# Kernel tuning notes

Measured on AMD Instinct MI355X. Metric: run time of the kernel, lower is better.

Reference implementation:

```python
import jax, jax.numpy as jnp
import numpy as np
from jax import lax

SD = 16          # sample_duration
STRIDE = 16      # feat_stride
SCALES = (4, 8, 16)
RATIOS = (0.5, 1.0, 2.0)
PRE_NMS = 1000   # proposals kept before NMS (TEST config)
POST_NMS = 128   # proposals kept after NMS
NMS_TH = 0.7


def _anchors2d():
    base = 16.0
    ctr = (base - 1.0) / 2.0
    out = []
    for r in RATIOS:
        ws = np.round(np.sqrt(base * base / r))
        hs = np.round(ws * r)
        for s in SCALES:
            w, h = ws * s, hs * s
            out.append([ctr - (w - 1) / 2, ctr - (h - 1) / 2,
                        ctr + (w - 1) / 2, ctr + (h - 1) / 2])
    return np.asarray(out, np.float32)                       # (9, 4)


def _anchors3d():
    # tube anchors: (x1, y1, t1, x2, y2, t2), durations [SD, SD/2, SD/4]
    a2 = _anchors2d()
    out = []
    for d in (SD, SD // 2, SD // 4):
        for a in a2:
            out.append([a[0], a[1], 0.0, a[2], a[3], d - 1.0])
    return np.asarray(out, np.float32)                       # (27, 6)


def _shifted(anchors, H, W):
    k = anchors.shape[-1]
    sx = jnp.arange(W, dtype=jnp.float32) * STRIDE
    sy = jnp.arange(H, dtype=jnp.float32) * STRIDE
    if k == 4:
        sh = jnp.stack(jnp.broadcast_arrays(sx[None, :], sy[:, None],
                                            sx[None, :], sy[:, None]), -1)
    else:
        z = jnp.zeros((H, W), jnp.float32)
        sh = jnp.stack(jnp.broadcast_arrays(sx[None, :], sy[:, None], z,
                                            sx[None, :], sy[:, None], z), -1)
    return (sh[:, :, None, :] + jnp.asarray(anchors)[None, None]).reshape(-1, k)


def _decode(anchors, deltas):
    # deltas layout: (d_ctr..., d_logsize...); works for 2D (k=4) and 3D (k=6)
    nd = anchors.shape[-1] // 2
    lo, hi = anchors[..., :nd], anchors[..., nd:]
    size = hi - lo + 1.0
    ctr = lo + 0.5 * (size - 1.0)
    pctr = deltas[..., :nd] * size + ctr
    psize = jnp.exp(deltas[..., nd:]) * size
    return jnp.concatenate([pctr - 0.5 * (psize - 1.0),
                            pctr + 0.5 * (psize - 1.0)], -1)


def _iou(b, boxes):
    # b: (k,), boxes: (N, k); area/volume IoU with +1 pixel convention
    nd = boxes.shape[-1] // 2
    lo = jnp.maximum(b[:nd], boxes[:, :nd])
    hi = jnp.minimum(b[nd:], boxes[:, nd:])
    inter = jnp.prod(jnp.maximum(hi - lo + 1.0, 0.0), -1)
    va = jnp.prod(b[nd:] - b[:nd] + 1.0)
    vb = jnp.prod(boxes[:, nd:] - boxes[:, :nd] + 1.0, -1)
    return inter / (va + vb - inter)


def _nms(boxes):
    # boxes already sorted by descending score; greedy NMS, fixed output size
    N = boxes.shape[0]

    def body(i, c):
        supp, keep = c
        idx = jnp.argmax(~supp)                 # first unsuppressed box
        keep = keep.at[i].set(idx.astype(jnp.int32))
        supp = supp | (_iou(boxes[idx], boxes) > NMS_TH)
        supp = supp.at[idx].set(True)
        return supp, keep

    _, keep = lax.fori_loop(0, POST_NMS, body,
                            (jnp.zeros(N, bool), jnp.zeros(POST_NMS, jnp.int32)))
    return keep


def _proposals(scores, deltas, anchors, maxs):
    # scores (B,N), deltas (B,N,k), anchors (N,k), maxs (B,1,k)
    boxes = jnp.clip(_decode(anchors[None], deltas), 0.0, maxs)
    _, idx = lax.top_k(scores, PRE_NMS)
    bx = jnp.take_along_axis(boxes, idx[..., None], axis=1)   # (B,PRE,k)
    keep = jax.vmap(_nms)(bx)                                 # (B,POST)
    sel = jnp.take_along_axis(bx, keep[..., None], axis=1)    # (B,POST,k)
    bidx = jnp.broadcast_to(
        jnp.arange(sel.shape[0], dtype=sel.dtype)[:, None, None],
        sel.shape[:2] + (1,))
    return lax.stop_gradient(jnp.concatenate([bidx, sel], -1))


def setup_inputs() -> dict:
    k = jax.random.split(jax.random.key(0), 8)
    s = 0.01
    return {
        "base_feat": jax.random.normal(k[0], (1, 256, 16, 32, 32), jnp.float32),
        "im_info": jnp.array([[512.0, 512.0, 1.0]], jnp.float32),
        "gt_boxes": jax.random.uniform(k[1], (1, 5, 7), jnp.float32) * 100.0,
        "gt_rois": jax.random.uniform(k[2], (1, 5, 16, 5), jnp.float32) * 100.0,
        "W_conv": jax.random.normal(k[3], (512, 256, 3, 3, 3), jnp.float32) * s,
        "b_conv": jnp.zeros((512,), jnp.float32),
        "W_cls": jax.random.normal(k[4], (54, 512), jnp.float32) * s,
        "b_cls": jnp.zeros((54,), jnp.float32),
        "W_bbox": jax.random.normal(k[5], (162, 512), jnp.float32) * s,
        "b_bbox": jnp.zeros((162,), jnp.float32),
        "W_cls16": jax.random.normal(k[6], (18, 512), jnp.float32) * s,
        "b_cls16": jnp.zeros((18,), jnp.float32),
        "W_bbox16": jax.random.normal(k[7], (36, 512), jnp.float32) * s,
        "b_bbox16": jnp.zeros((36,), jnp.float32),
    }


def reference(base_feat, im_info, gt_boxes, gt_rois, W_conv, b_conv,
              W_cls, b_cls, W_bbox, b_bbox, W_cls16, b_cls16,
              W_bbox16, b_bbox16):
    B, _, T, H, W = base_feat.shape
    # RPN_Conv: 3x3x3 Conv3d + ReLU
    conv1 = jax.nn.relu(
        lax.conv_general_dilated(base_feat, W_conv, (1, 1, 1), "SAME",
                                 dimension_numbers=("NCDHW", "OIDHW", "NCDHW"))
        + b_conv[None, :, None, None, None])
    # 1x1x1 score / bbox heads (3D)
    cls3 = jnp.einsum("bcthw,oc->bothw", conv1, W_cls) + b_cls[None, :, None, None, None]
    bbox3 = jnp.einsum("bcthw,oc->bothw", conv1, W_bbox) + b_bbox[None, :, None, None, None]
    # permute(0,1,3,4,2).mean(4) == mean over the temporal axis
    feat2 = conv1.mean(axis=2)
    cls2 = jnp.einsum("bchw,oc->bohw", feat2, W_cls16) + b_cls16[None, :, None, None]
    bbox2 = jnp.einsum("bchw,oc->bohw", feat2, W_bbox16) + b_bbox16[None, :, None, None]
    # reshape(x,2) + softmax over dim 1; fg prob is the second half of channels
    fg3 = jax.nn.softmax(cls3.reshape(B, 2, 27, T, H, W), axis=1)[:, 1]  # (B,27,T,H,W)
    fg2 = jax.nn.softmax(cls2.reshape(B, 2, 9, H, W), axis=1)[:, 1]      # (B,9,H,W)
    # proposal layers consume detached tensors (torch .data)
    fg3, fg2, bbox3d, bbox2d = map(lax.stop_gradient, (fg3, fg2, bbox3, bbox2))
    # flatten position-major (h, w, anchor)
    sc3 = fg3.mean(axis=2).transpose(0, 2, 3, 1).reshape(B, -1)
    dl3 = bbox3d.mean(axis=2).reshape(B, 27, 6, H, W).transpose(0, 3, 4, 1, 2).reshape(B, -1, 6)
    sc2 = fg2.transpose(0, 2, 3, 1).reshape(B, -1)
    dl2 = bbox2d.reshape(B, 9, 4, H, W).transpose(0, 3, 4, 1, 2).reshape(B, -1, 4)
    imh, imw = im_info[:, 0][:, None], im_info[:, 1][:, None]
    sdm = jnp.full_like(imw, SD - 1.0)
    max3 = jnp.stack([imw - 1, imh - 1, sdm, imw - 1, imh - 1, sdm], -1)  # (B,1,6)
    max2 = jnp.stack([imw - 1, imh - 1, imw - 1, imh - 1], -1)            # (B,1,4)
    rois = _proposals(sc3, dl3, _shifted(_anchors3d(), H, W), max3)       # (B,POST,7)
    rois16 = _proposals(sc2, dl2, _shifted(_anchors2d(), H, W), max2)     # (B,POST,5)
    z = jnp.zeros((), jnp.float32)  # eval mode: all RPN losses are 0
    return rois, rois16, z, z, z, z
```

## Files before the change

kernel.cpp:

```cpp
#include <hip/hip_runtime.h>
#include <hip/hip_bf16.h>
#include <cfloat>
#include <cstdint>


#define T_DIM 16
#define H_DIM 32
#define W_DIM 32
#define NVOX  (T_DIM*H_DIM*W_DIM)
#define HW    (H_DIM*W_DIM)
#define CIN   256
#define COUT  512
#define PRE_NMS 1000
#define POST_NMS 128
#define NMS_TH 0.7f

typedef __attribute__((ext_vector_type(8))) short v8s;
typedef __attribute__((ext_vector_type(4))) float v4f;
typedef __attribute__((ext_vector_type(4))) int v4i;

#define MFMA_B16(A,B,C) __builtin_amdgcn_mfma_f32_16x16x32_bf16(A,B,C,0,0,0)

__device__ __forceinline__ short f2bf(float x) {
    unsigned u = __float_as_uint(x);
    u += 0x7FFFu + ((u >> 16) & 1u);
    return (short)(u >> 16);
}
__device__ __forceinline__ float bf2f(short s) {
    return __uint_as_float(((unsigned)(unsigned short)s) << 16);
}

__constant__ float c_ws[3] = {23.f, 16.f, 11.f};
__constant__ float c_hs[3] = {12.f, 16.f, 22.f};
__constant__ float c_sc[3] = {4.f, 8.f, 16.f};
__constant__ float c_depth[3] = {16.f, 8.f, 4.f};

__global__ void k_split_w(const float* __restrict__ W, short* __restrict__ A0,
                          short* __restrict__ A1, short* __restrict__ A2) {
    int i = blockIdx.x * 256 + threadIdx.x;
    int c7 = i & 7;
    int o = (i >> 3) & 511;
    int ko = (i >> 12) & 31;
    int tap = i >> 17;
    int c = ko * 8 + c7;
    float x = W[(o * 256 + c) * 27 + tap];
    short h = f2bf(x); float r = x - bf2f(h);
    short m = f2bf(r); float r2 = r - bf2f(m);
    short l = f2bf(r2);
    A0[i] = h; A1[i] = m; A2[i] = l;
}

__global__ void k_build_wcomb(const float* __restrict__ Wcls, const float* __restrict__ Wbb,
                              float* __restrict__ Wc) {
    int i = blockIdx.x * 256 + threadIdx.x;
    int o = i & 255;
    int c = i >> 8;
    float v = 0.f;
    if (o < 54) v = Wcls[o * 512 + c];
    else if (o < 216) v = Wbb[(o - 54) * 512 + c];
    Wc[i] = v;
}

#define SPLIT2(X0, X1, OH, OM, OL) {                                          \
    unsigned u0_ = __float_as_uint(X0), u1_ = __float_as_uint(X1);            \
    OH = (int)__builtin_amdgcn_perm(u1_, u0_, 0x07060302u);                   \
    float h0_ = __uint_as_float(u0_ & 0xFFFF0000u);                           \
    float h1_ = __uint_as_float(u1_ & 0xFFFF0000u);                           \
    float r0_ = (X0) - h0_, r1_ = (X1) - h1_;                                 \
    unsigned v0_ = __float_as_uint(r0_), v1_ = __float_as_uint(r1_);          \
    OM = (int)__builtin_amdgcn_perm(v1_, v0_, 0x07060302u);                   \
    float m0_ = __uint_as_float(v0_ & 0xFFFF0000u);                           \
    float m1_ = __uint_as_float(v1_ & 0xFFFF0000u);                           \
    float s0_ = r0_ - m0_, s1_ = r1_ - m1_;                                   \
    OL = (int)__builtin_amdgcn_perm(__float_as_uint(s1_),                     \
                                    __float_as_uint(s0_), 0x07060302u);       \
}

__global__ void k_split_i(const float* __restrict__ I, v4i* __restrict__ Ih,
                          v4i* __restrict__ Im, v4i* __restrict__ Il) {
    int t = blockIdx.x * 256 + threadIdx.x;
    int vox = t & 16383;
    int ck8 = t >> 14;
    const float* ip = I + ((size_t)ck8 << 3) * NVOX + vox;
    int h[4], m[4], l[4];
#pragma unroll
    for (int j = 0; j < 4; ++j) {
        float x0 = ip[(size_t)(2 * j) * NVOX];
        float x1 = ip[(size_t)(2 * j + 1) * NVOX];
        SPLIT2(x0, x1, h[j], m[j], l[j]);
    }
    Ih[t] = (v4i){h[0], h[1], h[2], h[3]};
    Im[t] = (v4i){m[0], m[1], m[2], m[3]};
    Il[t] = (v4i){l[0], l[1], l[2], l[3]};
}

#define CV_SHIFT(TAP) {                                                       \
    int kt_ = (TAP) / 9 - 1, kh_ = ((TAP) / 3) % 3 - 1, kw_ = (TAP) % 3 - 1;  \
    int tt_ = bt + kt_, hh_ = bh + kh_, ww_ = bw + kw_;                       \
    bVal = ((unsigned)tt_ < 16u) && ((unsigned)hh_ < 32u) && ((unsigned)ww_ < 32u); \
    bOff = bVal ? ((tt_ << 10) + (hh_ << 5) + ww_) : 0;                       \
}

#define CV_LOAD_BP(CK8B) {                                                    \
    const size_t bidx_ = (((size_t)((CK8B) + skh * 2)) << 14) + bOff;         \
    nh0 = Ih[bidx_]; nh1 = Ih[bidx_ + NVOX];                                  \
    nm0 = Im[bidx_]; nm1 = Im[bidx_ + NVOX];                                  \
    nl0 = Il[bidx_]; nl1 = Il[bidx_ + NVOX];                                  \
}

#define CV_SELECT_B() {                                                       \
    v4i z_ = (v4i){0, 0, 0, 0};                                               \
    pbh0 = bVal ? nh0 : z_; pbh1 = bVal ? nh1 : z_;                           \
    pbm0 = bVal ? nm0 : z_; pbm1 = bVal ? nm1 : z_;                           \
    pbl0 = bVal ? nl0 : z_; pbl1 = bVal ? nl1 : z_;                           \
}

#define LOAD_ASET(S) {                                                        \
    const size_t aB_ = (((size_t)((S) >> 3) * 32 + (((S) & 7) << 2)) << 12) + aLane; \
    ah0 = *(const v8s*)(A0 + aB_);       ah1 = *(const v8s*)(A0 + aB_ + 128); \
    ah2 = *(const v8s*)(A0 + aB_ + 256); ah3 = *(const v8s*)(A0 + aB_ + 384); \
    am0 = *(const v8s*)(A1 + aB_);       am1 = *(const v8s*)(A1 + aB_ + 128); \
    am2 = *(const v8s*)(A1 + aB_ + 256); am3 = *(const v8s*)(A1 + aB_ + 384); \
    al0 = *(const v8s*)(A2 + aB_);       al1 = *(const v8s*)(A2 + aB_ + 128); \
    al2 = *(const v8s*)(A2 + aB_ + 256); al3 = *(const v8s*)(A2 + aB_ + 384); \
}

#define COMPUTE() {                                                           \
    _Pragma("unroll")                                                         \
    for (int j = 0; j < 4; ++j) {                                             \
        v8s bb = *(const v8s*)(&Bsh[0][uB + j * 16]);                         \
        v8s bm = *(const v8s*)(&Bsh[1][uB + j * 16]);                         \
        v8s bl = *(const v8s*)(&Bsh[2][uB + j * 16]);                         \
        v4f a;                                                                \
        a = acc[0][j];                                                        \
        a = MFMA_B16(ah0, bb, a); a = MFMA_B16(ah0, bm, a);                   \
        a = MFMA_B16(am0, bb, a); a = MFMA_B16(ah0, bl, a);                   \
        a = MFMA_B16(am0, bm, a); a = MFMA_B16(al0, bb, a);                   \
        acc[0][j] = a;                                                        \
        a = acc[1][j];                                                        \
        a = MFMA_B16(ah1, bb, a); a = MFMA_B16(ah1, bm, a);                   \
        a = MFMA_B16(am1, bb, a); a = MFMA_B16(ah1, bl, a);                   \
        a = MFMA_B16(am1, bm, a); a = MFMA_B16(al1, bb, a);                   \
        acc[1][j] = a;                                                        \
        a = acc[2][j];                                                        \
        a = MFMA_B16(ah2, bb, a); a = MFMA_B16(ah2, bm, a);                   \
        a = MFMA_B16(am2, bb, a); a = MFMA_B16(ah2, bl, a);                   \
        a = MFMA_B16(am2, bm, a); a = MFMA_B16(al2, bb, a);                   \
        acc[2][j] = a;                                                        \
        a = acc[3][j];                                                        \
        a = MFMA_B16(ah3, bb, a); a = MFMA_B16(ah3, bm, a);                   \
        a = MFMA_B16(am3, bb, a); a = MFMA_B16(ah3, bl, a);                   \
        a = MFMA_B16(am3, bm, a); a = MFMA_B16(al3, bb, a);                   \
        acc[3][j] = a;                                                        \
    }                                                                         \
}

__global__ __launch_bounds__(256) void k_conv3d_mfma(
        const v4i* __restrict__ Ih, const v4i* __restrict__ Im,
        const v4i* __restrict__ Il, const short* __restrict__ A0,
        const short* __restrict__ A1, const short* __restrict__ A2,
        const float* __restrict__ bias, float* __restrict__ O) {
    __shared__ v4i Bsh[3][512];
    const int tid = threadIdx.x;
    const int o0 = blockIdx.y * 128;
    const int v0 = blockIdx.x * 128;
    const int lane = tid & 63;
    const int wv = tid >> 6;
    const int quad = lane >> 4, m16 = lane & 15;
    const int wo = (wv >> 1) * 64;
    const int wvx = (wv & 1) * 64;

    const int sa_o = tid >> 1, skh = tid & 1;
    const int uW0 = (skh * 2) * 128 + sa_o;
    const int uW1 = (skh * 2 + 1) * 128 + sa_o;

    const int vbase = v0 + sa_o;
    const int bt = vbase >> 10, bh = (vbase >> 5) & 31, bw = vbase & 31;

    const int uB = quad * 128 + wvx + m16;

    const size_t aLane = ((size_t)(o0 + wo + m16) << 3) + ((size_t)quad << 12);

    v4f acc[4][4];
#pragma unroll
    for (int i = 0; i < 4; i++)
#pragma unroll
        for (int j = 0; j < 4; j++) acc[i][j] = (v4f){0.f, 0.f, 0.f, 0.f};

    int bOff, bVal;
    v4i pbh0, pbh1, pbm0, pbm1, pbl0, pbl1;
    v4i nh0, nh1, nm0, nm1, nl0, nl1;
    v8s ah0, ah1, ah2, ah3, am0, am1, am2, am3, al0, al1, al2, al3;

    CV_SHIFT(0);
    CV_LOAD_BP(0);
    CV_SELECT_B();

    for (int s = 0; s < 216; ++s) {
        __syncthreads();
        Bsh[0][uW0] = pbh0; Bsh[0][uW1] = pbh1;
        Bsh[1][uW0] = pbm0; Bsh[1][uW1] = pbm1;
        Bsh[2][uW0] = pbl0; Bsh[2][uW1] = pbl1;
        __syncthreads();
        LOAD_ASET(s);
        {
            int s1 = s + 1;
            if (s1 < 216) {
                if ((s1 & 7) == 0) CV_SHIFT(s1 >> 3);
                CV_LOAD_BP((s1 & 7) << 2);
            }
        }
        COMPUTE();
        if (s + 1 < 216) CV_SELECT_B();
    }

#pragma unroll
    for (int i = 0; i < 4; ++i) {
#pragma unroll
        for (int r = 0; r < 4; ++r) {
            int o = o0 + wo + i * 16 + quad * 4 + r;
            float bo = bias[o];
            float* dst = O + (size_t)o * NVOX + v0 + wvx + m16;
#pragma unroll
            for (int j = 0; j < 4; ++j)
                dst[j * 16] = fmaxf(acc[i][j][r] + bo, 0.f);
        }
    }
}

__global__ __launch_bounds__(256) void k_gemm_logits3(const float* __restrict__ conv1,
                                                      const float* __restrict__ Wc,
                                                      float* __restrict__ L) {
    __shared__ float As[16][64];
    __shared__ float Bs[16][64];
    const int tid = threadIdx.x;
    const int o0 = blockIdx.y * 64;
    const int v0 = blockIdx.x * 64;
    const int ty = tid >> 4, tx = tid & 15;
    const int c_l = tid >> 4, e4 = (tid & 15) << 2;

    float acc[4][4];
#pragma unroll
    for (int i = 0; i < 4; i++)
#pragma unroll
        for (int j = 0; j < 4; j++) acc[i][j] = 0.f;

    for (int ck = 0; ck < 512; ck += 16) {
        __syncthreads();
        *(float4*)(&As[c_l][e4]) = *(const float4*)(Wc + ((size_t)(ck + c_l) << 8) + o0 + e4);
        *(float4*)(&Bs[c_l][e4]) = *(const float4*)(conv1 + ((size_t)(ck + c_l) << 14) + v0 + e4);
        __syncthreads();
#pragma unroll
        for (int k = 0; k < 16; ++k) {
            float a[4], b[4];
            *(float4*)(a) = *(const float4*)(&As[k][ty * 4]);
            *(float4*)(b) = *(const float4*)(&Bs[k][tx * 4]);
#pragma unroll
            for (int i = 0; i < 4; i++)
#pragma unroll
                for (int j = 0; j < 4; j++)
                    acc[i][j] = fmaf(a[i], b[j], acc[i][j]);
        }
    }
#pragma unroll
    for (int i = 0; i < 4; i++) {
        float* dst = L + (size_t)(o0 + ty * 4 + i) * NVOX + v0 + tx * 4;
        *(float4*)(dst) = *(const float4*)(&acc[i][0]);
    }
}

__global__ void k_sc3(const float* __restrict__ L, const float* __restrict__ b_cls,
                      float* __restrict__ sc3) {
    int i = blockIdx.x * 256 + threadIdx.x;
    if (i >= 27 * HW) return;
    int a = i >> 10, hw = i & 1023;
    float b0 = b_cls[a], b1 = b_cls[27 + a];
    const float* L0 = L + (size_t)a * NVOX + hw;
    const float* L1 = L + (size_t)(27 + a) * NVOX + hw;
    float s = 0.f;
    for (int t = 0; t < T_DIM; t++) {
        float x0 = L0[t * HW] + b0, x1 = L1[t * HW] + b1;
        float m = fmaxf(x0, x1);
        float e0 = expf(x0 - m), e1 = expf(x1 - m);
        s += e1 / (e0 + e1);
    }
    sc3[hw * 27 + a] = s * (1.f / 16.f);
}

__global__ void k_dl3(const float* __restrict__ L, const float* __restrict__ b_bbox,
                      float* __restrict__ dl3) {
    int i = blockIdx.x * 256 + threadIdx.x;
    if (i >= 162 * HW) return;
    int ch = i >> 10, hw = i & 1023;
    const float* Lr = L + (size_t)(54 + ch) * NVOX + hw;
    float s = 0.f;
    for (int t = 0; t < T_DIM; t++) s += Lr[t * HW];
    s = s * (1.f / 16.f) + b_bbox[ch];
    int a = ch / 6, d = ch - a * 6;
    dl3[((size_t)hw * 27 + a) * 6 + d] = s;
}

__global__ void k_feat2(const float* __restrict__ conv1, float* __restrict__ feat2) {
    int i = blockIdx.x * 256 + threadIdx.x;
    int c = i >> 10, hw = i & 1023;
    const float* src = conv1 + (size_t)c * NVOX + hw;
    float s = 0.f;
    for (int t = 0; t < T_DIM; t++) s += src[t * HW];
    feat2[i] = s * (1.f / 16.f);
}

__global__ void k_gemm2d(const float* __restrict__ feat2, const float* __restrict__ Wcls16,
                         const float* __restrict__ Wbb16, float* __restrict__ L2) {
    int g = blockIdx.x * 256 + threadIdx.x;
    int o = g >> 10, hw = g & 1023;
    const float* wrow = (o < 18) ? (Wcls16 + (size_t)o * 512) : (Wbb16 + (size_t)(o - 18) * 512);
    float s = 0.f;
    for (int c = 0; c < 512; c++) s = fmaf(wrow[c], feat2[(size_t)c * HW + hw], s);
    L2[(size_t)o * HW + hw] = s;
}

__global__ void k_sc2(const float* __restrict__ L2, const float* __restrict__ b_cls16,
                      float* __restrict__ sc2) {
    int i = blockIdx.x * 256 + threadIdx.x;
    if (i >= 9 * HW) return;
    int a = i >> 10, hw = i & 1023;
    float x0 = L2[(size_t)a * HW + hw] + b_cls16[a];
    float x1 = L2[(size_t)(9 + a) * HW + hw] + b_cls16[9 + a];
    float m = fmaxf(x0, x1);
    float e0 = expf(x0 - m), e1 = expf(x1 - m);
    sc2[hw * 9 + a] = e1 / (e0 + e1);
}

__global__ void k_dl2(const float* __restrict__ L2, const float* __restrict__ b_bbox16,
                      float* __restrict__ dl2) {
    int i = blockIdx.x * 256 + threadIdx.x;
    if (i >= 36 * HW) return;
    int ch = i >> 10, hw = i & 1023;
    float v = L2[(size_t)(18 + ch) * HW + hw] + b_bbox16[ch];
    int a = ch >> 2, d = ch & 3;
    dl2[((size_t)hw * 9 + a) * 4 + d] = v;
}

__device__ __forceinline__ unsigned mapf(float f) {
    unsigned u = __float_as_uint(f);
    return (u & 0x80000000u) ? ~u : (u | 0x80000000u);
}

__global__ __launch_bounds__(1024) void k_proposal(const float* __restrict__ im_info,
                                                   const float* __restrict__ sc3,
                                                   const float* __restrict__ dl3,
                                                   const float* __restrict__ sc2,
                                                   const float* __restrict__ dl2,
                                                   float* __restrict__ out) {
    const int branch = blockIdx.x;
    const int tid = threadIdx.x;
    const int A = (branch == 0) ? 27 : 9;
    const int nd = (branch == 0) ? 3 : 2;
    const float* scores = (branch == 0) ? sc3 : sc2;
    const float* deltas = (branch == 0) ? dl3 : dl2;
    const int K = PRE_NMS;
    const int ept = A;
    const int base = tid * ept;

    __shared__ unsigned hist[256];
    __shared__ unsigned long long keys[1024];
    __shared__ float bx[PRE_NMS][6];
    __shared__ int keep[POST_NMS];
    __shared__ unsigned wsum[16];
    __shared__ unsigned long long alive[16];
    __shared__ int sh_b, sh_next, bcast;

    unsigned prefix = 0;
    int rank = K;
    for (int shift = 24; shift >= 0; shift -= 8) {
        if (tid < 256) hist[tid] = 0;
        __syncthreads();
        const unsigned mask_hi = (shift == 24) ? 0u : (0xFFFFFFFFu << (shift + 8));
        for (int j = 0; j < ept; j++) {
            unsigned m = mapf(scores[base + j]);
            if ((m & mask_hi) == prefix)
                atomicAdd(&hist[(m >> shift) & 255], 1u);
        }
        __syncthreads();
        for (int d = 1; d < 256; d <<= 1) {
            unsigned add = 0;
            if (tid < 256 && tid + d < 256) add = hist[tid + d];
            __syncthreads();
            if (tid < 256) hist[tid] += add;
            __syncthreads();
        }
        if (tid < 256) {
            bool win = (hist[tid] >= (unsigned)rank) &&
                       (tid == 255 || hist[tid + 1] < (unsigned)rank);
            if (win) { sh_b = tid; sh_next = (tid == 255) ? 0 : (int)hist[tid + 1]; }
        }
        __syncthreads();
        prefix |= (unsigned)sh_b << shift;
        rank -= sh_next;
        __syncthreads();
    }
    const unsigned tau = prefix;

    int gt_c = 0, eq_c = 0;
    for (int j = 0; j < ept; j++) {
        unsigned m = mapf(scores[base + j]);
        gt_c += (m > tau);
        eq_c += (m == tau);
    }
    unsigned cnt = ((unsigned)gt_c << 16) | (unsigned)eq_c;
    const int lane = tid & 63, wid = tid >> 6;
    unsigned x = cnt;
    for (int d = 1; d < 64; d <<= 1) {
        unsigned y = __shfl_up(x, d);
        if (lane >= d) x += y;
    }
    if (lane == 63) wsum[wid] = x;
    __syncthreads();
    if (wid == 0) {
        unsigned w = (lane < 16) ? wsum[lane] : 0;
        for (int d = 1; d < 16; d <<= 1) {
            unsigned y = __shfl_up(w, d);
            if (lane >= d) w += y;
        }
        if (lane < 16) wsum[lane] = w;
    }
    __syncthreads();
    unsigned excl = x - cnt + (wid ? wsum[wid - 1] : 0);
    const int c1 = (int)(wsum[15] >> 16);
    int gi = (int)(excl >> 16);
    int ei = (int)(excl & 0xFFFFu);
    for (int j = 0; j < ept; j++) {
        int idx = base + j;
        unsigned m = mapf(scores[idx]);
        unsigned long long key = ((unsigned long long)m << 32) |
                                 (unsigned)(0xFFFFFFFFu - (unsigned)idx);
        if (m > tau) {
            keys[gi++] = key;
        } else if (m == tau) {
            if (c1 + ei < K) keys[c1 + ei] = key;
            ei++;
        }
    }
    if (tid < 1024 - K) keys[K + tid] = 0;
    __syncthreads();

    for (int k = 2; k <= 1024; k <<= 1) {
        for (int j = k >> 1; j > 0; j >>= 1) {
            int ixj = tid ^ j;
            if (ixj > tid) {
                unsigned long long a = keys[tid], b = keys[ixj];
                bool sw2 = ((tid & k) == 0) ? (a < b) : (a > b);
                if (sw2) { keys[tid] = b; keys[ixj] = a; }
            }
            __syncthreads();
        }
    }

    const float imh = im_info[0], imw = im_info[1];
    if (tid < K) {
        int n = (int)(0xFFFFFFFFu - (unsigned)(keys[tid] & 0xFFFFFFFFull));
        int cell = n / A, a = n - cell * A;
        int hc = cell >> 5, wc = cell & 31;
        int a2 = (branch == 0) ? (a % 9) : a;
        int ri = a2 / 3, si = a2 % 3;
        float w = c_ws[ri] * c_sc[si], h = c_hs[ri] * c_sc[si];
        float lo[3], hi[3], mx[3];
        lo[0] = 7.5f - (w - 1.f) * 0.5f + 16.f * wc;
        hi[0] = 7.5f + (w - 1.f) * 0.5f + 16.f * wc;
        mx[0] = imw - 1.f;
        lo[1] = 7.5f - (h - 1.f) * 0.5f + 16.f * hc;
        hi[1] = 7.5f + (h - 1.f) * 0.5f + 16.f * hc;
        mx[1] = imh - 1.f;
        if (branch == 0) { lo[2] = 0.f; hi[2] = c_depth[a / 9] - 1.f; mx[2] = (float)(T_DIM - 1); }
        const float* dp = deltas + (size_t)n * (2 * nd);
        for (int d = 0; d < nd; d++) {
            float size = hi[d] - lo[d] + 1.f;
            float ctr = lo[d] + 0.5f * (size - 1.f);
            float pctr = dp[d] * size + ctr;
            float psize = expf(dp[nd + d]) * size;
            float pl = pctr - 0.5f * (psize - 1.f);
            float ph = pctr + 0.5f * (psize - 1.f);
            bx[tid][d]      = fminf(fmaxf(pl, 0.f), mx[d]);
            bx[tid][nd + d] = fminf(fmaxf(ph, 0.f), mx[d]);
        }
    }
    if (tid < 16) alive[tid] = (tid < 15) ? ~0ull : ((1ull << (K - 15 * 64)) - 1);
    __syncthreads();

    float myb[6]; float myvol = 1.f;
    if (tid < K) {
        for (int d = 0; d < 6; d++) myb[d] = bx[tid][d];
        for (int d = 0; d < nd; d++) myvol *= (myb[nd + d] - myb[d] + 1.f);
    }
    for (int i = 0; i < POST_NMS; ++i) {
        if (tid < 64) {
            unsigned long long wvb = (tid < 16) ? alive[tid] : 0ull;
            int cand = wvb ? (tid * 64 + __ffsll(wvb) - 1) : 0x7fffffff;
#pragma unroll
            for (int off = 32; off; off >>= 1)
                cand = min(cand, __shfl_xor(cand, off));
            if (tid == 0) {
                int m = (cand == 0x7fffffff) ? 0 : cand;
                bcast = m; keep[i] = m;
            }
        }
        __syncthreads();
        int sel = bcast;
        bool s = false;
        if (tid < K) {
            float inter = 1.f, selvol = 1.f;
            for (int d = 0; d < nd; d++) {
                float slo = bx[sel][d], shi = bx[sel][nd + d];
                float l = fmaxf(slo, myb[d]);
                float hh = fminf(shi, myb[nd + d]);
                inter *= fmaxf(hh - l + 1.f, 0.f);
                selvol *= (shi - slo + 1.f);
            }
            float iou = inter / (selvol + myvol - inter);
            s = (iou > NMS_TH) || (tid == sel);
        }
        unsigned long long bal = __ballot(s);
        if (lane == 0 && bal) alive[wid] &= ~bal;
        __syncthreads();
    }

    if (tid < POST_NMS) {
        int k = keep[tid];
        if (branch == 0) {
            float* o = out + (size_t)tid * 7;
            o[0] = 0.f;
            for (int d = 0; d < 6; d++) o[1 + d] = bx[k][d];
        } else {
            float* o = out + 128 * 7 + (size_t)tid * 5;
            o[0] = 0.f;
            for (int d = 0; d < 4; d++) o[1 + d] = bx[k][d];
        }
    }
    if (branch == 0 && tid == 0) {
        out[1536] = 0.f; out[1537] = 0.f; out[1538] = 0.f; out[1539] = 0.f;
    }
}

extern "C" void kernel_launch(void* const* d_in, const int* in_sizes, int n_in,
                              void* d_out, int out_size, void* d_ws, size_t ws_size,
                              hipStream_t stream) {
    (void)in_sizes; (void)n_in; (void)out_size; (void)ws_size;
    const float* base_feat = (const float*)d_in[0];
    const float* im_info   = (const float*)d_in[1];
    const float* W_conv    = (const float*)d_in[4];
    const float* b_conv    = (const float*)d_in[5];
    const float* W_cls     = (const float*)d_in[6];
    const float* b_cls     = (const float*)d_in[7];
    const float* W_bbox    = (const float*)d_in[8];
    const float* b_bbox    = (const float*)d_in[9];
    const float* W_cls16   = (const float*)d_in[10];
    const float* b_cls16   = (const float*)d_in[11];
    const float* W_bbox16  = (const float*)d_in[12];
    const float* b_bbox16  = (const float*)d_in[13];
    float* out = (float*)d_out;

    char* ws = (char*)d_ws;
    const size_t AW = (size_t)27 * 512 * 256;
    short* A0 = (short*)ws;
    short* A1 = A0 + AW;
    short* A2 = A1 + AW;
    float* L3 = (float*)ws;
    size_t off = AW * 3 * sizeof(short);
    float* Wcomb  = (float*)(ws + off); off += (size_t)512 * 256 * 4;
    float* conv1  = (float*)(ws + off); off += (size_t)COUT * NVOX * 4;
    float* feat2  = (float*)(ws + off); off += (size_t)512 * HW * 4;
    float* L2     = (float*)(ws + off); off += (size_t)64 * HW * 4;
    float* sc3    = (float*)(ws + off); off += (size_t)27 * HW * 4;
    float* dl3    = (float*)(ws + off); off += (size_t)27 * HW * 6 * 4;
    float* sc2    = (float*)(ws + off); off += (size_t)9 * HW * 4;
    float* dl2    = (float*)(ws + off); off += (size_t)9 * HW * 4 * 4;
    v4i* Ih = (v4i*)(ws + off); off += (size_t)32 * NVOX * 16;
    v4i* Im_ = (v4i*)(ws + off); off += (size_t)32 * NVOX * 16;
    v4i* Il = (v4i*)(ws + off); off += (size_t)32 * NVOX * 16;

    k_split_w<<<13824, 256, 0, stream>>>(W_conv, A0, A1, A2);
    k_build_wcomb<<<512, 256, 0, stream>>>(W_cls, W_bbox, Wcomb);
    k_split_i<<<2048, 256, 0, stream>>>(base_feat, Ih, Im_, Il);
    {
        dim3 g(NVOX / 128, COUT / 128);
        k_conv3d_mfma<<<g, 256, 0, stream>>>(Ih, Im_, Il, A0, A1, A2, b_conv, conv1);
    }
    {
        dim3 g(NVOX / 64, 4);
        k_gemm_logits3<<<g, 256, 0, stream>>>(conv1, Wcomb, L3);
    }
    k_sc3<<<(27 * HW + 255) / 256, 256, 0, stream>>>(L3, b_cls, sc3);
    k_dl3<<<(162 * HW + 255) / 256, 256, 0, stream>>>(L3, b_bbox, dl3);
    k_feat2<<<(512 * HW) / 256, 256, 0, stream>>>(conv1, feat2);
    k_gemm2d<<<(54 * HW) / 256, 256, 0, stream>>>(feat2, W_cls16, W_bbox16, L2);
    k_sc2<<<(9 * HW + 255) / 256, 256, 0, stream>>>(L2, b_cls16, sc2);
    k_dl2<<<(36 * HW + 255) / 256, 256, 0, stream>>>(L2, b_bbox16, dl2);
    k_proposal<<<2, 1024, 0, stream>>>(im_info, sc3, dl3, sc2, dl2, out);
}
```

Measured before the change: 950.1 us.

## Double-buffer conv3d B tile in LDS and A fragments in registers

The conv3d MFMA loop is restructured to ping-pong two LDS buffers for the im2col B tile and two register sets for the weight A fragments. This needs only one __syncthreads per step instead of two. The next step's A fragments and the B tile are prefetched while the current step's MFMAs run, to hide global and LDS latency. Launch bounds now request 2 blocks per CU. The cost is more LDS and doubled A-fragment registers, which raises spill or occupancy risk.

```diff
diff --git a/kernel.cpp b/kernel.cpp
--- a/kernel.cpp
+++ b/kernel.cpp
@@ -108,59 +108,77 @@
     nl0 = Il[bidx_]; nl1 = Il[bidx_ + NVOX];                                  \
 }
 
-#define CV_SELECT_B() {                                                       \
-    v4i z_ = (v4i){0, 0, 0, 0};                                               \
-    pbh0 = bVal ? nh0 : z_; pbh1 = bVal ? nh1 : z_;                           \
-    pbm0 = bVal ? nm0 : z_; pbm1 = bVal ? nm1 : z_;                           \
-    pbl0 = bVal ? nl0 : z_; pbl1 = bVal ? nl1 : z_;                           \
-}
-
-#define LOAD_ASET(S) {                                                        \
+#define LOAD_ASET_M(S, H0,H1,H2,H3, M0,M1,M2,M3, L0,L1,L2,L3) {               \
     const size_t aB_ = (((size_t)((S) >> 3) * 32 + (((S) & 7) << 2)) << 12) + aLane; \
-    ah0 = *(const v8s*)(A0 + aB_);       ah1 = *(const v8s*)(A0 + aB_ + 128); \
-    ah2 = *(const v8s*)(A0 + aB_ + 256); ah3 = *(const v8s*)(A0 + aB_ + 384); \
-    am0 = *(const v8s*)(A1 + aB_);       am1 = *(const v8s*)(A1 + aB_ + 128); \
-    am2 = *(const v8s*)(A1 + aB_ + 256); am3 = *(const v8s*)(A1 + aB_ + 384); \
-    al0 = *(const v8s*)(A2 + aB_);       al1 = *(const v8s*)(A2 + aB_ + 128); \
-    al2 = *(const v8s*)(A2 + aB_ + 256); al3 = *(const v8s*)(A2 + aB_ + 384); \
-}
-
-#define COMPUTE() {                                                           \
+    H0 = *(const v8s*)(A0 + aB_);       H1 = *(const v8s*)(A0 + aB_ + 128);   \
+    H2 = *(const v8s*)(A0 + aB_ + 256); H3 = *(const v8s*)(A0 + aB_ + 384);   \
+    M0 = *(const v8s*)(A1 + aB_);       M1 = *(const v8s*)(A1 + aB_ + 128);   \
+    M2 = *(const v8s*)(A1 + aB_ + 256); M3 = *(const v8s*)(A1 + aB_ + 384);   \
+    L0 = *(const v8s*)(A2 + aB_);       L1 = *(const v8s*)(A2 + aB_ + 128);   \
+    L2 = *(const v8s*)(A2 + aB_ + 256); L3 = *(const v8s*)(A2 + aB_ + 384);   \
+}
+
+#define COMPUTE_M(BUF, H0,H1,H2,H3, M0,M1,M2,M3, L0,L1,L2,L3) {               \
     _Pragma("unroll")                                                         \
     for (int j = 0; j < 4; ++j) {                                             \
-        v8s bb = *(const v8s*)(&Bsh[0][uB + j * 16]);                         \
-        v8s bm = *(const v8s*)(&Bsh[1][uB + j * 16]);                         \
-        v8s bl = *(const v8s*)(&Bsh[2][uB + j * 16]);                         \
+        v8s bb = *(const v8s*)(&Bsh[BUF][0][uB + j * 16]);                    \
+        v8s bm = *(const v8s*)(&Bsh[BUF][1][uB + j * 16]);                    \
+        v8s bl = *(const v8s*)(&Bsh[BUF][2][uB + j * 16]);                    \
         v4f a;                                                                \
         a = acc[0][j];                                                        \
-        a = MFMA_B16(ah0, bb, a); a = MFMA_B16(ah0, bm, a);                   \
-        a = MFMA_B16(am0, bb, a); a = MFMA_B16(ah0, bl, a);                   \
-        a = MFMA_B16(am0, bm, a); a = MFMA_B16(al0, bb, a);                   \
+        a = MFMA_B16(H0, bb, a); a = MFMA_B16(H0, bm, a);                     \
+        a = MFMA_B16(M0, bb, a); a = MFMA_B16(H0, bl, a);                     \
+        a = MFMA_B16(M0, bm, a); a = MFMA_B16(L0, bb, a);                     \
         acc[0][j] = a;                                                        \
         a = acc[1][j];                                                        \
-        a = MFMA_B16(ah1, bb, a); a = MFMA_B16(ah1, bm, a);                   \
-        a = MFMA_B16(am1, bb, a); a = MFMA_B16(ah1, bl, a);                   \
-        a = MFMA_B16(am1, bm, a); a = MFMA_B16(al1, bb, a);                   \
+        a = MFMA_B16(H1, bb, a); a = MFMA_B16(H1, bm, a);                     \
+        a = MFMA_B16(M1, bb, a); a = MFMA_B16(H1, bl, a);                     \
+        a = MFMA_B16(M1, bm, a); a = MFMA_B16(L1, bb, a);                     \
         acc[1][j] = a;                                                        \
         a = acc[2][j];                                                        \
-        a = MFMA_B16(ah2, bb, a); a = MFMA_B16(ah2, bm, a);                   \
-        a = MFMA_B16(am2, bb, a); a = MFMA_B16(ah2, bl, a);                   \
-        a = MFMA_B16(am2, bm, a); a = MFMA_B16(al2, bb, a);                   \
+        a = MFMA_B16(H2, bb, a); a = MFMA_B16(H2, bm, a);                     \
+        a = MFMA_B16(M2, bb, a); a = MFMA_B16(H2, bl, a);                     \
+        a = MFMA_B16(M2, bm, a); a = MFMA_B16(L2, bb, a);                     \
         acc[2][j] = a;                                                        \
         a = acc[3][j];                                                        \
-        a = MFMA_B16(ah3, bb, a); a = MFMA_B16(ah3, bm, a);                   \
-        a = MFMA_B16(am3, bb, a); a = MFMA_B16(ah3, bl, a);                   \
-        a = MFMA_B16(am3, bm, a); a = MFMA_B16(al3, bb, a);                   \
+        a = MFMA_B16(H3, bb, a); a = MFMA_B16(H3, bm, a);                     \
+        a = MFMA_B16(M3, bb, a); a = MFMA_B16(H3, bl, a);                     \
+        a = MFMA_B16(M3, bm, a); a = MFMA_B16(L3, bb, a);                     \
         acc[3][j] = a;                                                        \
     }                                                                         \
 }
 
-__global__ __launch_bounds__(256) void k_conv3d_mfma(
+#define LOAD_ASET(S, ...) LOAD_ASET_M(S, __VA_ARGS__)
+#define COMPUTE(BUF, ...) COMPUTE_M(BUF, __VA_ARGS__)
+
+#define ASET(P) P##h0,P##h1,P##h2,P##h3,P##m0,P##m1,P##m2,P##m3,P##l0,P##l1,P##l2,P##l3
+
+#define ITER_BODY(SS, BUF, CUR, ALT) {                                        \
+    int s1_ = (SS) + 1, s2_ = (SS) + 2;                                       \
+    if (s1_ < 216) { LOAD_ASET(s1_, ASET(ALT)); }                             \
+    if (s1_ < 216) {                                                          \
+        v4i z_ = (v4i){0, 0, 0, 0};                                           \
+        Bsh[(BUF) ^ 1][0][uW0] = bValCur ? nh0 : z_;                          \
+        Bsh[(BUF) ^ 1][0][uW1] = bValCur ? nh1 : z_;                          \
+        Bsh[(BUF) ^ 1][1][uW0] = bValCur ? nm0 : z_;                          \
+        Bsh[(BUF) ^ 1][1][uW1] = bValCur ? nm1 : z_;                          \
+        Bsh[(BUF) ^ 1][2][uW0] = bValCur ? nl0 : z_;                          \
+        Bsh[(BUF) ^ 1][2][uW1] = bValCur ? nl1 : z_;                          \
+    }                                                                         \
+    if (s2_ < 216) {                                                          \
+        if ((s2_ & 7) == 0) CV_SHIFT(s2_ >> 3);                               \
+        CV_LOAD_BP((s2_ & 7) << 2);                                           \
+        bValCur = bVal;                                                       \
+    }                                                                         \
+    COMPUTE(BUF, ASET(CUR));                                                  \
+}
+
+__global__ __launch_bounds__(256, 2) void k_conv3d_mfma(
         const v4i* __restrict__ Ih, const v4i* __restrict__ Im,
         const v4i* __restrict__ Il, const short* __restrict__ A0,
         const short* __restrict__ A1, const short* __restrict__ A2,
         const float* __restrict__ bias, float* __restrict__ O) {
-    __shared__ v4i Bsh[3][512];
+    __shared__ v4i Bsh[2][3][512];
     const int tid = threadIdx.x;
     const int o0 = blockIdx.y * 128;
     const int v0 = blockIdx.x * 128;
@@ -187,31 +205,32 @@
 #pragma unroll
         for (int j = 0; j < 4; j++) acc[i][j] = (v4f){0.f, 0.f, 0.f, 0.f};
 
-    int bOff, bVal;
-    v4i pbh0, pbh1, pbm0, pbm1, pbl0, pbl1;
+    int bOff, bVal, bValCur;
     v4i nh0, nh1, nm0, nm1, nl0, nl1;
-    v8s ah0, ah1, ah2, ah3, am0, am1, am2, am3, al0, al1, al2, al3;
+    v8s Ph0, Ph1, Ph2, Ph3, Pm0, Pm1, Pm2, Pm3, Pl0, Pl1, Pl2, Pl3;
+    v8s Qh0, Qh1, Qh2, Qh3, Qm0, Qm1, Qm2, Qm3, Ql0, Ql1, Ql2, Ql3;
 
     CV_SHIFT(0);
+    bValCur = bVal;
     CV_LOAD_BP(0);
-    CV_SELECT_B();
-
-    for (int s = 0; s < 216; ++s) {
-        __syncthreads();
-        Bsh[0][uW0] = pbh0; Bsh[0][uW1] = pbh1;
-        Bsh[1][uW0] = pbm0; Bsh[1][uW1] = pbm1;
-        Bsh[2][uW0] = pbl0; Bsh[2][uW1] = pbl1;
-        __syncthreads();
-        LOAD_ASET(s);
-        {
-            int s1 = s + 1;
-            if (s1 < 216) {
-                if ((s1 & 7) == 0) CV_SHIFT(s1 >> 3);
-                CV_LOAD_BP((s1 & 7) << 2);
-            }
-        }
-        COMPUTE();
-        if (s + 1 < 216) CV_SELECT_B();
+    {
+        v4i z_ = (v4i){0, 0, 0, 0};
+        Bsh[0][0][uW0] = bValCur ? nh0 : z_;
+        Bsh[0][0][uW1] = bValCur ? nh1 : z_;
+        Bsh[0][1][uW0] = bValCur ? nm0 : z_;
+        Bsh[0][1][uW1] = bValCur ? nm1 : z_;
+        Bsh[0][2][uW0] = bValCur ? nl0 : z_;
+        Bsh[0][2][uW1] = bValCur ? nl1 : z_;
+    }
+    CV_LOAD_BP(4);
+    LOAD_ASET(0, ASET(P));
+    __syncthreads();
+
+    for (int s = 0; s < 216; s += 2) {
+        ITER_BODY(s, 0, P, Q);
+        __syncthreads();
+        ITER_BODY(s + 1, 1, Q, P);
+        __syncthreads();
     }
 
 #pragma unroll
```

New measurement: 936.2 us. Within noise of the previous version (-1.5%).
